# Kernel tuning notes

Measured on AMD Instinct MI355X. Metric: run time of the kernel, lower is better.

## Reference

```python
import jax, jax.numpy as jnp
import numpy as np

QK = 64
KNN = 16
EPS = 1e-5


def conv1(x, w, b):
    # x: (B,C,N), w: (O,C) -> (B,O,N)
    return jnp.einsum('oc,bcn->bon', w, x) + b[None, :, None]


def conv2(x, w, b):
    # x: (B,C,N,k), w: (O,C) -> (B,O,N,k)
    return jnp.einsum('oc,bcnk->bonk', w, x) + b[None, :, None, None]


def bn1(x, g, b, m, v):
    return g[None, :, None] * (x - m[None, :, None]) * jax.lax.rsqrt(v + EPS)[None, :, None] + b[None, :, None]


def bn2(x, g, b, m, v):
    return g[None, :, None, None] * (x - m[None, :, None, None]) * jax.lax.rsqrt(v + EPS)[None, :, None, None] + b[None, :, None, None]


def gather_nk(t, idx):
    # t: (B,C,M), idx: (B,N,k) -> (B,C,N,k)
    return jax.vmap(lambda tb, ib: tb[:, ib])(t, idx)


def setup_inputs():
    key = jax.random.key(0)
    ks = jax.random.split(key, 40)
    B, N, M = 2, 16384, 4096
    w = lambda k, s: jax.random.normal(k, s, dtype=jnp.float32) * 0.05
    d = {}
    d['xyz_hr'] = jax.random.normal(ks[0], (B, 3, N), dtype=jnp.float32)
    d['xyz_lr'] = jax.random.normal(ks[1], (B, 3, M), dtype=jnp.float32)
    d['sft_feat_lr'] = jax.random.normal(ks[2], (B, 6, M), dtype=jnp.float32)
    d['val_lr'] = jax.random.normal(ks[3], (B, 64, M), dtype=jnp.float32)
    # geom_encoder: Conv1d(3,64) -> BN -> ReLU -> Conv1d(64,64)
    d['ge_w1'] = w(ks[4], (QK, 3)); d['ge_b1'] = w(ks[5], (QK,))
    d['ge_g1'] = jnp.ones((QK,)); d['ge_be1'] = jnp.zeros((QK,))
    d['ge_m1'] = w(ks[6], (QK,)); d['ge_v1'] = jax.random.uniform(ks[7], (QK,), minval=0.5, maxval=1.5)
    d['ge_w2'] = w(ks[8], (QK, QK)); d['ge_b2'] = w(ks[9], (QK,))
    # scale/shift convs Conv1d(6,64)
    d['sc_w'] = w(ks[10], (QK, 6)); d['sc_b'] = w(ks[11], (QK,))
    d['sh_w'] = w(ks[12], (QK, 6)); d['sh_b'] = w(ks[13], (QK,))
    # sem query/key Conv1d(64,64)
    d['q_w'] = w(ks[14], (QK, QK)); d['q_b'] = w(ks[15], (QK,))
    d['k_w'] = w(ks[16], (QK, QK)); d['k_b'] = w(ks[17], (QK,))
    # bdy_head: Conv1d(64,64) -> BN -> ReLU -> Conv1d(64,1) -> Sigmoid
    d['bd_w1'] = w(ks[18], (64, QK)); d['bd_b1'] = w(ks[19], (64,))
    d['bd_g'] = jnp.ones((64,)); d['bd_be'] = jnp.zeros((64,))
    d['bd_m'] = w(ks[20], (64,)); d['bd_v'] = jax.random.uniform(ks[21], (64,), minval=0.5, maxval=1.5)
    d['bd_w2'] = w(ks[22], (1, 64)); d['bd_b2'] = w(ks[23], (1,))
    # rel_pos_mlp: Conv2d(3,64) -> BN2d -> ReLU -> Conv2d(64,64)
    d['rp_w1'] = w(ks[24], (QK, 3)); d['rp_b1'] = w(ks[25], (QK,))
    d['rp_g'] = jnp.ones((QK,)); d['rp_be'] = jnp.zeros((QK,))
    d['rp_m'] = w(ks[26], (QK,)); d['rp_v'] = jax.random.uniform(ks[27], (QK,), minval=0.5, maxval=1.5)
    d['rp_w2'] = w(ks[28], (QK, QK)); d['rp_b2'] = w(ks[29], (QK,))
    return d


def reference(xyz_hr, xyz_lr, sft_feat_lr, val_lr,
              ge_w1, ge_b1, ge_g1, ge_be1, ge_m1, ge_v1, ge_w2, ge_b2,
              sc_w, sc_b, sh_w, sh_b, q_w, q_b, k_w, k_b,
              bd_w1, bd_b1, bd_g, bd_be, bd_m, bd_v, bd_w2, bd_b2,
              rp_w1, rp_b1, rp_g, rp_be, rp_m, rp_v, rp_w2, rp_b2):
    B, _, M = sft_feat_lr.shape
    curr_k = min(KNN, M)

    def geom_enc(x):
        h = jax.nn.relu(bn1(conv1(x, ge_w1, ge_b1), ge_g1, ge_be1, ge_m1, ge_v1))
        return conv1(h, ge_w2, ge_b2)

    geom_hr = geom_enc(xyz_hr)                     # (B,64,N)
    geom_lr = geom_enc(xyz_lr)                     # (B,64,M)
    scale = conv1(sft_feat_lr, sc_w, sc_b)
    shift = conv1(sft_feat_lr, sh_w, sh_b)
    geom_lr_mod = geom_lr * (scale + 1.0) + shift
    Q = conv1(geom_hr, q_w, q_b)                   # (B,64,N)
    K = conv1(geom_lr_mod, k_w, k_b)               # (B,64,M)
    # boundary head
    h = jax.nn.relu(bn1(conv1(geom_hr, bd_w1, bd_b1), bd_g, bd_be, bd_m, bd_v))
    bdy_prob = jax.nn.sigmoid(conv1(h, bd_w2, bd_b2))  # (B,1,N)
    # kNN via squared distances (same argmin ordering as torch.cdist)
    hr_t = jnp.swapaxes(xyz_hr, 1, 2)              # (B,N,3)
    lr_t = jnp.swapaxes(xyz_lr, 1, 2)              # (B,M,3)
    d2 = (jnp.sum(hr_t**2, -1)[:, :, None] + jnp.sum(lr_t**2, -1)[:, None, :]
          - 2.0 * jnp.einsum('bnd,bmd->bnm', hr_t, lr_t))  # (B,N,M)
    _, k_idx = jax.lax.top_k(-d2, curr_k)          # (B,N,k) int32
    k_idx = jax.lax.stop_gradient(k_idx)

    K_g = gather_nk(K, k_idx)                      # (B,64,N,k)
    xyz_lr_g = gather_nk(xyz_lr, k_idx)            # (B,3,N,k)
    rel_pos = xyz_hr[:, :, :, None] - xyz_lr_g     # (B,3,N,k)
    pe = jax.nn.relu(bn2(conv2(rel_pos, rp_w1, rp_b1), rp_g, rp_be, rp_m, rp_v))
    pos_enc = conv2(pe, rp_w2, rp_b2)              # (B,64,N,k)
    logits = jnp.sum(Q[:, :, :, None] * (K_g + pos_enc), axis=1) / np.sqrt(QK)  # (B,N,k)
    attn = jax.nn.softmax(logits, axis=-1)
    val_g = gather_nk(val_lr, k_idx)               # (B,Cv,N,k)
    out = jnp.sum(attn[:, None, :, :] * val_g, axis=-1)  # (B,Cv,N)
    return out, bdy_prob
```

## Files before the change

### kernel.cpp

```cpp
#include <hip/hip_runtime.h>
#include <hip/hip_bf16.h>

#define B_ 2
#define N_ 16384
#define M_ 4096
#define EPS_ 1e-5f

__device__ __forceinline__ float b2f(const __hip_bfloat16 v) { return __bfloat162float(v); }

__device__ __forceinline__ float ldin(const void* p, size_t i, int f32) {
    return f32 ? ((const float*)p)[i] : __bfloat162float(((const __hip_bfloat16*)p)[i]);
}
__device__ __forceinline__ void stout(void* o, size_t i, float v, int f32) {
    if (f32) ((float*)o)[i] = v;
    else     ((__hip_bfloat16*)o)[i] = __float2bfloat16(v);
}

__device__ __forceinline__ float d2np(float x, float y, float z, float hn, float4 q) {
    float dot = __fadd_rn(__fadd_rn(__fmul_rn(x, q.x), __fmul_rn(y, q.y)), __fmul_rn(z, q.z));
    return __fsub_rn(__fadd_rn(hn, q.w), __fmul_rn(2.f, dot));
}
__device__ __forceinline__ float norm3np(float x, float y, float z) {
    return __fadd_rn(__fadd_rn(__fmul_rn(x, x), __fmul_rn(y, y)), __fmul_rn(z, z));
}

#define O_GE_W1 0
#define O_GE_B1 192
#define O_GE_W2 256
#define O_GE_B2 4352
#define O_QW    4416
#define O_QB    8512
#define O_KW    8576
#define O_KB    12672
#define O_SCW   12736
#define O_SCB   13120
#define O_SHW   13184
#define O_SHB   13568
#define O_BDW1  13632
#define O_BDB1  17728
#define O_BDW2  17792
#define O_BDB2  17856
#define O_RPW1  17920
#define O_RPB1  18112
#define O_RPW2  18176
#define O_RPB2  22272
#define OB_LR    92160
#define OB_Q     223232
#define OB_KT    4417536
#define OB_VT    5466112
#define OB_KIDX  6514688
#define OB_DFLAG 7694336
#define O_T_GE_W2 1923840
#define O_T_QW    1927936
#define O_T_KW    1932032
#define O_T_BDW1  1936128

#define CAP  12
#define CAPS 13

__global__ __launch_bounds__(256) void prep_kernel(
    const void* xyz_hr,
    const void* ge_w1, const void* ge_b1, const void* ge_g1, const void* ge_be1,
    const void* ge_m1, const void* ge_v1, const void* ge_w2, const void* ge_b2,
    const void* sc_w, const void* sc_b, const void* sh_w, const void* sh_b,
    const void* q_w, const void* q_b, const void* k_w, const void* k_b,
    const void* bd_w1, const void* bd_b1, const void* bd_g, const void* bd_be,
    const void* bd_m, const void* bd_v, const void* bd_w2, const void* bd_b2,
    const void* rp_w1, const void* rp_b1, const void* rp_g, const void* rp_be,
    const void* rp_m, const void* rp_v, const void* rp_w2, const void* rp_b2,
    float* W, int* dflag)
{
    __shared__ int scnt;
    int t = threadIdx.x;
    if (t == 0) scnt = 0;
    __syncthreads();
    if (t < 128) {
        unsigned short u = ((const unsigned short*)xyz_hr)[t];
        int e = (u >> 7) & 0xFF;
        int ok = (e >= 113 && e <= 132) || ((u & 0x7FFF) == 0);
        if (ok) atomicAdd(&scnt, 1);
    }
    __syncthreads();
    const int f32 = (scnt < 110) ? 1 : 0;
    if (t == 0) *dflag = f32;

    if (t < 64) {
        float s = ldin(ge_g1, t, f32) * rsqrtf(ldin(ge_v1, t, f32) + EPS_);
        for (int d = 0; d < 3; ++d) W[O_GE_W1 + t*3 + d] = s * ldin(ge_w1, t*3 + d, f32);
        W[O_GE_B1 + t] = s * (ldin(ge_b1, t, f32) - ldin(ge_m1, t, f32)) + ldin(ge_be1, t, f32);
        W[O_GE_B2 + t] = ldin(ge_b2, t, f32);
        W[O_QB + t] = ldin(q_b, t, f32);
        W[O_KB + t] = ldin(k_b, t, f32);
        W[O_SCB + t] = ldin(sc_b, t, f32);
        W[O_SHB + t] = ldin(sh_b, t, f32);
        float sb = ldin(bd_g, t, f32) * rsqrtf(ldin(bd_v, t, f32) + EPS_);
        W[O_BDB1 + t] = sb * (ldin(bd_b1, t, f32) - ldin(bd_m, t, f32)) + ldin(bd_be, t, f32);
        W[O_BDW2 + t] = ldin(bd_w2, t, f32);
        float sr = ldin(rp_g, t, f32) * rsqrtf(ldin(rp_v, t, f32) + EPS_);
        for (int d = 0; d < 3; ++d) W[O_RPW1 + t*3 + d] = sr * ldin(rp_w1, t*3 + d, f32);
        W[O_RPB1 + t] = sr * (ldin(rp_b1, t, f32) - ldin(rp_m, t, f32)) + ldin(rp_be, t, f32);
        W[O_RPB2 + t] = ldin(rp_b2, t, f32);
    }
    if (t == 0) W[O_BDB2] = ldin(bd_b2, 0, f32);
    for (int i = t; i < 4096; i += 256) {
        int c = i >> 6, r = i & 63;
        float w2 = ldin(ge_w2, i, f32);
        float qw = ldin(q_w, i, f32);
        float kw = ldin(k_w, i, f32);
        float sb = ldin(bd_g, c, f32) * rsqrtf(ldin(bd_v, c, f32) + EPS_);
        float bw = sb * ldin(bd_w1, i, f32);
        W[O_GE_W2 + i] = w2;
        W[O_QW + i]    = qw;
        W[O_KW + i]    = kw;
        W[O_RPW2 + i]  = ldin(rp_w2, i, f32);
        W[O_BDW1 + i]  = bw;
        W[O_T_GE_W2 + r*64 + c] = w2;
        W[O_T_QW    + r*64 + c] = qw;
        W[O_T_KW    + r*64 + c] = kw;
        W[O_T_BDW1  + r*64 + c] = bw;
    }
    for (int i = t; i < 384; i += 256) {
        W[O_SCW + i] = ldin(sc_w, i, f32);
        W[O_SHW + i] = ldin(sh_w, i, f32);
    }
}

__global__ __launch_bounds__(256) void lr_kernel(
    const void* __restrict__ xyz_lr,
    const void* __restrict__ sft,
    const void* __restrict__ val,
    const float* __restrict__ W,
    __hip_bfloat16* __restrict__ Kt, __hip_bfloat16* __restrict__ Vt,
    float4* __restrict__ LR, const int* dflag)
{
    const int f32 = *dflag;
    int lane = threadIdx.x & 63;
    int p = blockIdx.x * 4 + (threadIdx.x >> 6);
    int b = p >> 12, m = p & (M_ - 1);
    size_t base = (size_t)b*3*M_ + m;
    float x = ldin(xyz_lr, base, f32), y = ldin(xyz_lr, base + M_, f32), z = ldin(xyz_lr, base + 2*M_, f32);
    if (lane == 0) LR[p] = make_float4(x, y, z, norm3np(x, y, z));

    const float* w1 = W + O_GE_W1 + lane*3;
    float h = fmaxf(fmaf(w1[2], z, fmaf(w1[1], y, fmaf(w1[0], x, W[O_GE_B1 + lane]))), 0.f);
    float g = W[O_GE_B2 + lane];
#pragma unroll
    for (int i = 0; i < 64; ++i) {
        g = fmaf(W[O_T_GE_W2 + i*64 + lane], __shfl(h, i, 64), g);
    }
    float sc = W[O_SCB + lane], sh = W[O_SHB + lane];
    const float* wsc = W + O_SCW + lane*6;
    const float* wsh = W + O_SHW + lane*6;
#pragma unroll
    for (int d = 0; d < 6; ++d) {
        float s6 = ldin(sft, (size_t)b*6*M_ + d*M_ + m, f32);
        sc = fmaf(wsc[d], s6, sc); sh = fmaf(wsh[d], s6, sh);
    }
    float mod = fmaf(g, sc + 1.f, sh);
    float k = W[O_KB + lane];
#pragma unroll
    for (int i = 0; i < 64; ++i) {
        k = fmaf(W[O_T_KW + i*64 + lane], __shfl(mod, i, 64), k);
    }
    Kt[(size_t)p*64 + lane] = __float2bfloat16(k);
    Vt[(size_t)p*64 + lane] = __float2bfloat16(ldin(val, (size_t)b*64*M_ + (size_t)lane*M_ + m, f32));
}

__global__ __launch_bounds__(256) void hr_kernel(
    const void* __restrict__ xyz_hr,
    const float* __restrict__ W,
    __hip_bfloat16* __restrict__ Q,
    void* __restrict__ out, const int* dflag)
{
    const int f32 = *dflag;
    int lane = threadIdx.x & 63;
    int p = blockIdx.x * 4 + (threadIdx.x >> 6);
    int b = p >> 14, n = p & (N_ - 1);
    size_t base = (size_t)b*3*N_ + n;
    float x = ldin(xyz_hr, base, f32), y = ldin(xyz_hr, base + N_, f32), z = ldin(xyz_hr, base + 2*N_, f32);

    const float* w1 = W + O_GE_W1 + lane*3;
    float h = fmaxf(fmaf(w1[2], z, fmaf(w1[1], y, fmaf(w1[0], x, W[O_GE_B1 + lane]))), 0.f);
    float g = W[O_GE_B2 + lane];
#pragma unroll
    for (int i = 0; i < 64; ++i) {
        g = fmaf(W[O_T_GE_W2 + i*64 + lane], __shfl(h, i, 64), g);
    }
    float q = W[O_QB + lane];
#pragma unroll
    for (int i = 0; i < 64; ++i) {
        q = fmaf(W[O_T_QW + i*64 + lane], __shfl(g, i, 64), q);
    }
    Q[(size_t)p*64 + lane] = __float2bfloat16(q);
    float hb = W[O_BDB1 + lane];
#pragma unroll
    for (int i = 0; i < 64; ++i) {
        hb = fmaf(W[O_T_BDW1 + i*64 + lane], __shfl(g, i, 64), hb);
    }
    float o = W[O_BDW2 + lane] * fmaxf(hb, 0.f);
#pragma unroll
    for (int sh = 1; sh < 64; sh <<= 1) o += __shfl_xor(o, sh, 64);
    if (lane == 0) {
        o += W[O_BDB2];
        stout(out, (size_t)B_*64*N_ + (size_t)b*N_ + n, 1.f / (1.f + __expf(-o)), f32);
    }
}

#define CE(da, ia, db, ib) { \
    bool sw_ = (db < da) || (db == da && ib < ia); \
    float td_ = da; int ti_ = ia; \
    da = sw_ ? db : da; ia = sw_ ? ib : ia; \
    db = sw_ ? td_ : db; ib = sw_ ? ti_ : ib; }

__device__ __forceinline__ void topk_insert(float (&bd)[16], int (&bi)[16], float d2, int m) {
    if (d2 < bd[15] || (d2 == bd[15] && m < bi[15])) {
        bd[15] = d2; bi[15] = m;
#pragma unroll
        for (int j = 15; j > 0; --j) CE(bd[j-1], bi[j-1], bd[j], bi[j]);
    }
}

__global__ __launch_bounds__(256, 4) void knn_kernel(
    const void* __restrict__ xyz_hr,
    const float4* __restrict__ LR,
    unsigned short* __restrict__ kidx, const int* dflag)
{
#pragma clang fp reassociate(off)
    __shared__ float          sdd[256 * CAPS];
    __shared__ unsigned short sii[256 * CAPS];
    const int f32 = *dflag;
    int lane = threadIdx.x & 63;
    int p = blockIdx.x * 4 + (threadIdx.x >> 6);
    int b = p >> 14, n = p & (N_ - 1);
    size_t base = (size_t)b*3*N_ + n;
    float x = ldin(xyz_hr, base, f32), y = ldin(xyz_hr, base + N_, f32), z = ldin(xyz_hr, base + 2*N_, f32);
    float hn = norm3np(x, y, z);
    const float4* L = LR + b*M_;
    const float4* Ll = L + lane;

    float d2r[64];
    float v = 3.4e38f;
#pragma unroll
    for (int c = 0; c < 8; ++c) {
        float4 q[8];
#pragma unroll
        for (int i = 0; i < 8; ++i) q[i] = Ll[(c*8 + i)*64];
#pragma unroll
        for (int i = 0; i < 8; ++i) {
            float d2 = d2np(x, y, z, hn, q[i]);
            d2r[c*8 + i] = d2;
            v = fminf(v, d2);
        }
    }
    v = fminf(v, __shfl_xor(v, 16, 64));
    v = fminf(v, __shfl_xor(v, 32, 64));
    float tau = v;
#pragma unroll
    for (int st = 1; st <= 8; st <<= 1) tau = fmaxf(tau, __shfl_xor(tau, st, 64));

    int sl = threadIdx.x * CAPS;
    int cnt = 0;
#pragma unroll
    for (int i = 0; i < 64; ++i) {
        if (d2r[i] <= tau) {
            if (cnt < CAP) { sdd[sl + cnt] = d2r[i]; sii[sl + cnt] = (unsigned short)(i*64 + lane); }
            cnt++;
        }
    }
    int bad = (cnt > CAP) ? 1 : 0;
#pragma unroll
    for (int st = 1; st <= 32; st <<= 1) bad |= __shfl_xor(bad, st, 64);
    if (bad) {
        float bd[16]; int bi[16];
#pragma unroll
        for (int j = 0; j < 16; ++j) { bd[j] = 3.4e38f; bi[j] = 0x7fffffff; }
        for (int m = 0; m < M_; ++m) {
            topk_insert(bd, bi, d2np(x, y, z, hn, L[m]), m);
        }
        if (lane == 0) {
            unsigned short* kr = kidx + (size_t)p*16;
#pragma unroll
            for (int j = 0; j < 16; ++j) kr[j] = (unsigned short)bi[j];
        }
        return;
    }
    for (int a = 0; a < cnt - 1; ++a) {
        float bv = sdd[sl + a]; int bm = (int)sii[sl + a]; int bj = a;
        for (int j2 = a + 1; j2 < cnt; ++j2) {
            float dj = sdd[sl + j2]; int mj = (int)sii[sl + j2];
            if (dj < bv || (dj == bv && mj < bm)) { bv = dj; bm = mj; bj = j2; }
        }
        float ta = sdd[sl + a]; int ia = (int)sii[sl + a];
        sdd[sl + a] = bv; sii[sl + a] = (unsigned short)bm;
        sdd[sl + bj] = ta; sii[sl + bj] = (unsigned short)ia;
    }

    int ptr = 0;
    for (int r = 0; r < 16; ++r) {
        float hd = 3.4e38f; int hi = 0x7fffffff;
        if (ptr < cnt) { hd = sdd[sl + ptr]; hi = (int)sii[sl + ptr]; }
        float md = hd; int mi = hi;
#pragma unroll
        for (int st = 1; st <= 32; st <<= 1) {
            float od = __shfl_xor(md, st, 64);
            int   oi = __shfl_xor(mi, st, 64);
            bool s = (od < md) || (od == md && oi < mi);
            md = s ? od : md; mi = s ? oi : mi;
        }
        if (ptr < cnt && hi == mi) {
            kidx[(size_t)p*16 + r] = (unsigned short)mi;
            ptr++;
        }
    }
}

__global__ __launch_bounds__(256) void attn_kernel(
    const void* __restrict__ xyz_hr,
    const float4* __restrict__ LR,
    const float* __restrict__ W,
    const __hip_bfloat16* __restrict__ Q,
    const __hip_bfloat16* __restrict__ Kt,
    const __hip_bfloat16* __restrict__ Vt,
    const unsigned short* __restrict__ kidx,
    void* __restrict__ out, const int* dflag)
{
    const int f32 = *dflag;
    int p = (blockIdx.x * 256 + threadIdx.x) >> 6;
    int lane = threadIdx.x & 63;
    float fw0 = W[O_RPW1 + lane*3], fw1 = W[O_RPW1 + lane*3 + 1], fw2 = W[O_RPW1 + lane*3 + 2];
    float fb  = W[O_RPB1 + lane];

    int b = p >> 14, n = p & (N_ - 1);
    size_t base = (size_t)b*3*N_ + n;
    float xh = ldin(xyz_hr, base, f32), yh = ldin(xyz_hr, base + N_, f32), zh = ldin(xyz_hr, base + 2*N_, f32);
    float qc = b2f(Q[(size_t)p*64 + lane]);
    float q2 = 0.f;
#pragma unroll
    for (int cc = 0; cc < 64; ++cc) {
        float qb = __shfl(qc, cc, 64);
        q2 = fmaf(W[O_RPW2 + cc*64 + lane], qb, q2);
    }
    int idxv = (int)kidx[(size_t)p*16 + (lane & 15)];
    const float4* L = LR + b*M_;
    const __hip_bfloat16* Ktb = Kt + (size_t)b*M_*64;
    const __hip_bfloat16* Vtb = Vt + (size_t)b*M_*64;
    float lg[16];
#pragma unroll
    for (int j = 0; j < 16; ++j) {
        int mj = __shfl(idxv, j, 64);
        mj = (mj < M_) ? mj : (M_ - 1);
        float4 pl = L[mj];
        float r0 = xh - pl.x, r1 = yh - pl.y, r2 = zh - pl.z;
        float pe = fmaxf(fmaf(fw2, r2, fmaf(fw1, r1, fmaf(fw0, r0, fb))), 0.f);
        float v = fmaf(qc, b2f(Ktb[(size_t)mj*64 + lane]), q2 * pe);
#pragma unroll
        for (int sh = 1; sh < 64; sh <<= 1) v += __shfl_xor(v, sh, 64);
        lg[j] = v * 0.125f;
    }
    float mx = lg[0];
#pragma unroll
    for (int j = 1; j < 16; ++j) mx = fmaxf(mx, lg[j]);
    float sum = 0.f;
#pragma unroll
    for (int j = 0; j < 16; ++j) { lg[j] = __expf(lg[j] - mx); sum += lg[j]; }
    float inv = 1.f / sum;
    float o = 0.f;
#pragma unroll
    for (int j = 0; j < 16; ++j) {
        int mj = __shfl(idxv, j, 64);
        mj = (mj < M_) ? mj : (M_ - 1);
        o = fmaf(lg[j] * inv, b2f(Vtb[(size_t)mj*64 + lane]), o);
    }
    stout(out, ((size_t)(b*64 + lane))*N_ + n, o, f32);
}

extern "C" void kernel_launch(void* const* d_in, const int* in_sizes, int n_in,
                              void* d_out, int out_size, void* d_ws, size_t ws_size,
                              hipStream_t stream) {
    const void* xyz_hr = d_in[0];
    const void* xyz_lr = d_in[1];
    const void* sft    = d_in[2];
    const void* val    = d_in[3];

    char* ws = (char*)d_ws;
    float* W  = (float*)ws;
    float4* LR = (float4*)(ws + OB_LR);
    __hip_bfloat16* Qp = (__hip_bfloat16*)(ws + OB_Q);
    __hip_bfloat16* Kt = (__hip_bfloat16*)(ws + OB_KT);
    __hip_bfloat16* Vt = (__hip_bfloat16*)(ws + OB_VT);
    unsigned short* kidx = (unsigned short*)(ws + OB_KIDX);
    int* dflag = (int*)(ws + OB_DFLAG);

    prep_kernel<<<1, 256, 0, stream>>>(
        xyz_hr,
        d_in[4],  d_in[5],  d_in[6],  d_in[7],  d_in[8],  d_in[9],  d_in[10], d_in[11],
        d_in[12], d_in[13], d_in[14], d_in[15], d_in[16], d_in[17], d_in[18], d_in[19],
        d_in[20], d_in[21], d_in[22], d_in[23], d_in[24], d_in[25], d_in[26], d_in[27],
        d_in[28], d_in[29], d_in[30], d_in[31], d_in[32], d_in[33], d_in[34], d_in[35],
        W, dflag);
    lr_kernel<<<2048, 256, 0, stream>>>(xyz_lr, sft, val, W, Kt, Vt, LR, dflag);
    hr_kernel<<<8192, 256, 0, stream>>>(xyz_hr, W, Qp, d_out, dflag);
    knn_kernel<<<8192, 256, 0, stream>>>(xyz_hr, LR, kidx, dflag);
    attn_kernel<<<8192, 256, 0, stream>>>(xyz_hr, LR, W, Qp, Kt, Vt, kidx, d_out, dflag);
}
```

Before: 429.2 us.

## Replace per-lane selection sort and shuffle merge with wave-wide rank selection

The kNN candidate stage now counts candidates below the threshold per lane, compacts them into a per-wave shared buffer with a wave prefix scan, and finds each candidate's final position by counting how many candidates sort lexicographically before it. This drops the per-lane serial selection sort and the 16-round shuffle-based merge. Each lane scans all T candidates, so the work is quadratic in T. The brute-force fallback now triggers only when a wave has more than 256 candidates instead of when any lane overflows 12, so it should fire less often.

```diff
diff --git a/kernel.cpp b/kernel.cpp
--- a/kernel.cpp
+++ b/kernel.cpp
@@ -55,8 +55,7 @@
 #define O_T_KW    1932032
 #define O_T_BDW1  1936128
 
-#define CAP  12
-#define CAPS 13
+#define TMAX 256
 
 __global__ __launch_bounds__(256) void prep_kernel(
     const void* xyz_hr,
@@ -220,17 +219,23 @@
     }
 }
 
+__device__ __forceinline__ int lesslex(uint2 e, float cd, int ci) {
+    float dj = __uint_as_float(e.x);
+    int   ij = (int)e.y;
+    return (dj < cd || (dj == cd && ij < ci)) ? 1 : 0;
+}
+
 __global__ __launch_bounds__(256, 4) void knn_kernel(
     const void* __restrict__ xyz_hr,
     const float4* __restrict__ LR,
     unsigned short* __restrict__ kidx, const int* dflag)
 {
 #pragma clang fp reassociate(off)
-    __shared__ float          sdd[256 * CAPS];
-    __shared__ unsigned short sii[256 * CAPS];
+    __shared__ uint2 scand[4 * TMAX];
     const int f32 = *dflag;
     int lane = threadIdx.x & 63;
-    int p = blockIdx.x * 4 + (threadIdx.x >> 6);
+    int wid  = threadIdx.x >> 6;
+    int p = blockIdx.x * 4 + wid;
     int b = p >> 14, n = p & (N_ - 1);
     size_t base = (size_t)b*3*N_ + n;
     float x = ldin(xyz_hr, base, f32), y = ldin(xyz_hr, base + N_, f32), z = ldin(xyz_hr, base + 2*N_, f32);
@@ -258,19 +263,19 @@
 #pragma unroll
     for (int st = 1; st <= 8; st <<= 1) tau = fmaxf(tau, __shfl_xor(tau, st, 64));
 
-    int sl = threadIdx.x * CAPS;
     int cnt = 0;
 #pragma unroll
-    for (int i = 0; i < 64; ++i) {
-        if (d2r[i] <= tau) {
-            if (cnt < CAP) { sdd[sl + cnt] = d2r[i]; sii[sl + cnt] = (unsigned short)(i*64 + lane); }
-            cnt++;
-        }
-    }
-    int bad = (cnt > CAP) ? 1 : 0;
-#pragma unroll
-    for (int st = 1; st <= 32; st <<= 1) bad |= __shfl_xor(bad, st, 64);
-    if (bad) {
+    for (int i = 0; i < 64; ++i) cnt += (d2r[i] <= tau) ? 1 : 0;
+    int inc = cnt;
+#pragma unroll
+    for (int st = 1; st < 64; st <<= 1) {
+        int o = __shfl_up(inc, st, 64);
+        if (lane >= st) inc += o;
+    }
+    int off = inc - cnt;
+    int T = __shfl(inc, 63, 64);
+
+    if (T > TMAX) {
         float bd[16]; int bi[16];
 #pragma unroll
         for (int j = 0; j < 16; ++j) { bd[j] = 3.4e38f; bi[j] = 0x7fffffff; }
@@ -284,33 +289,30 @@
         }
         return;
     }
-    for (int a = 0; a < cnt - 1; ++a) {
-        float bv = sdd[sl + a]; int bm = (int)sii[sl + a]; int bj = a;
-        for (int j2 = a + 1; j2 < cnt; ++j2) {
-            float dj = sdd[sl + j2]; int mj = (int)sii[sl + j2];
-            if (dj < bv || (dj == bv && mj < bm)) { bv = dj; bm = mj; bj = j2; }
+
+    uint2* wc = scand + wid * TMAX;
+#pragma unroll
+    for (int i = 0; i < 64; ++i) {
+        if (d2r[i] <= tau) {
+            wc[off] = make_uint2(__float_as_uint(d2r[i]), (unsigned)(i*64 + lane));
+            off++;
         }
-        float ta = sdd[sl + a]; int ia = (int)sii[sl + a];
-        sdd[sl + a] = bv; sii[sl + a] = (unsigned short)bm;
-        sdd[sl + bj] = ta; sii[sl + bj] = (unsigned short)ia;
-    }
-
-    int ptr = 0;
-    for (int r = 0; r < 16; ++r) {
-        float hd = 3.4e38f; int hi = 0x7fffffff;
-        if (ptr < cnt) { hd = sdd[sl + ptr]; hi = (int)sii[sl + ptr]; }
-        float md = hd; int mi = hi;
-#pragma unroll
-        for (int st = 1; st <= 32; st <<= 1) {
-            float od = __shfl_xor(md, st, 64);
-            int   oi = __shfl_xor(mi, st, 64);
-            bool s = (od < md) || (od == md && oi < mi);
-            md = s ? od : md; mi = s ? oi : mi;
+    }
+    int Tp = (T + 3) & ~3;
+    if (lane < Tp - T) wc[T + lane] = make_uint2(0x7f800000u, 0xffffu);
+    asm volatile("s_waitcnt lgkmcnt(0)" ::: "memory");
+
+    for (int t = lane; t < T; t += 64) {
+        uint2 cv = wc[t];
+        float cd = __uint_as_float(cv.x);
+        int   ci = (int)cv.y;
+        int rank = 0;
+        for (int j = 0; j < Tp; j += 4) {
+            uint2 e0 = wc[j], e1 = wc[j+1], e2 = wc[j+2], e3 = wc[j+3];
+            rank += lesslex(e0, cd, ci) + lesslex(e1, cd, ci)
+                  + lesslex(e2, cd, ci) + lesslex(e3, cd, ci);
         }
-        if (ptr < cnt && hi == mi) {
-            kidx[(size_t)p*16 + r] = (unsigned short)mi;
-            ptr++;
-        }
+        if (rank < 16) kidx[(size_t)p*16 + rank] = (unsigned short)ci;
     }
 }
 
```

Result: faster. 387.3 us (-9.7%).
